# Optimization experiments

Measured on AMD Instinct MI355X. Metric: run time of the kernel, lower is better.

## Reference

```python
import jax, jax.numpy as jnp
import numpy as np

N_S, N_C, N_L = 100000, 20000, 5000
E_U, E_T = 2000000, 500000
D_S, D_C, D_L, H = 64, 32, 128, 128
N_LAYERS = 3  # num_layers=2 -> ModuleList holds 3 hetero layers


def _sage(h_src, h_dst, src_idx, dst_idx, W_self, W_neigh, b, n_dst):
    # DGL SAGEConv 'mean': fc_self(h_dst) + fc_neigh(mean of in-neighbor src feats) + bias
    summed = jax.ops.segment_sum(h_src[src_idx], dst_idx, num_segments=n_dst)  # [n_dst, d]
    deg = jax.ops.segment_sum(jnp.ones((src_idx.shape[0],), h_src.dtype), dst_idx, num_segments=n_dst)
    h_neigh = summed / jnp.maximum(deg, 1.0)[:, None]
    return h_dst @ W_self + h_neigh @ W_neigh + b


def setup_inputs() -> dict:
    key = jax.random.key(0)
    ks = jax.random.split(key, 24)
    s = 0.05
    inp = {
        'feat_student': jax.random.normal(ks[0], (N_S, D_S), jnp.float32),
        'feat_concept': jax.random.normal(ks[1], (N_C, D_C), jnp.float32),
        'feat_lecture': jax.random.normal(ks[2], (N_L, D_L), jnp.float32),
        'W_fs': jax.random.normal(ks[3], (D_S, H), jnp.float32) * s,
        'b_fs': jnp.zeros((H,), jnp.float32),
        'W_fc': jax.random.normal(ks[4], (D_C, H), jnp.float32) * s,
        'b_fc': jnp.zeros((H,), jnp.float32),
        'W_fl': jax.random.normal(ks[5], (D_L, H), jnp.float32) * s,
        'b_fl': jnp.zeros((H,), jnp.float32),
        # per-layer, per-relation SAGE params (all dims 128 so they stack)
        'W_self_u': jax.random.normal(ks[6], (N_LAYERS, H, H), jnp.float32) * s,
        'W_neigh_u': jax.random.normal(ks[7], (N_LAYERS, H, H), jnp.float32) * s,
        'b_u': jnp.zeros((N_LAYERS, H), jnp.float32),
        'W_self_t': jax.random.normal(ks[8], (N_LAYERS, H, H), jnp.float32) * s,
        'W_neigh_t': jax.random.normal(ks[9], (N_LAYERS, H, H), jnp.float32) * s,
        'b_t': jnp.zeros((N_LAYERS, H), jnp.float32),
        'und_src': jax.random.randint(ks[10], (E_U,), 0, N_S, jnp.int32),
        'und_dst': jax.random.randint(ks[11], (E_U,), 0, N_C, jnp.int32),
        'tea_src': jax.random.randint(ks[12], (E_T,), 0, N_L, jnp.int32),
        'tea_dst': jax.random.randint(ks[13], (E_T,), 0, N_C, jnp.int32),
    }
    return inp


def reference(feat_student, feat_concept, feat_lecture,
              W_fs, b_fs, W_fc, b_fc, W_fl, b_fl,
              W_self_u, W_neigh_u, b_u, W_self_t, W_neigh_t, b_t,
              und_src, und_dst, tea_src, tea_dst):
    # input projections per node type
    h_s = feat_student @ W_fs + b_fs
    h_c = feat_concept @ W_fc + b_fc
    h_l = feat_lecture @ W_fl + b_fl
    n_c = h_c.shape[0]
    for i in range(N_LAYERS):
        ou = _sage(h_s, h_c, und_src, und_dst, W_self_u[i], W_neigh_u[i], b_u[i], n_c)
        ot = _sage(h_l, h_c, tea_src, tea_dst, W_self_t[i], W_neigh_t[i], b_t[i], n_c)
        # HeteroGraphConv cross-relation aggregate: 'mean' on layer 0, default 'sum' after
        h_c = (ou + ot) * (0.5 if i == 0 else 1.0)
        if i != N_LAYERS - 1:
            h_c = jax.nn.relu(h_c)  # dropout is identity in eval mode
        # student/lecture are never destination types -> features pass through
    return h_c  # [N_C, 128] concept embeddings
```

## Files before the change

kernel.cpp:

```cpp
#include <hip/hip_runtime.h>
#include <hip/hip_bf16.h>
#include <cstdint>
#include <cstddef>

#define NS_ 100000
#define NC_ 20000
#define NL_ 5000
#define EU_ 2000000
#define ET_ 500000
#define H_  128

#define NBK_ 625
#define CHK_ 1954
#define UBLK_ 1024
#define TBLK_ 256
#define CAPU_ 3600
#define CAPT_ 1024
#define SEDGE_ 3712
#define SROW_ 640

typedef __attribute__((ext_vector_type(8))) short bs8;
typedef __attribute__((ext_vector_type(4))) float f32x4;
typedef __attribute__((ext_vector_type(2))) float v2f;

__device__ inline short bf_rne(float f) {
    unsigned u = __float_as_uint(f);
    u = (u + 0x7fffu + ((u >> 16) & 1u)) >> 16;
    return (short)u;
}
__device__ inline unsigned pack_bf16x2(float a, float b) {
    return ((unsigned)(unsigned short)bf_rne(a)) |
           (((unsigned)(unsigned short)bf_rne(b)) << 16);
}
__device__ inline float bflo(unsigned w) { return __uint_as_float(w << 16); }
__device__ inline float bfhi(unsigned w) { return __uint_as_float(w & 0xffff0000u); }

#define B_SCU UBLK_
#define B_SCT TBLK_
#define B_SCAT (B_SCU + B_SCT)
#define B_CVT 512
#define B_PACK 480
#define B_BC 2
#define B_WFC 16

__global__ __launch_bounds__(256) void count_kernel(
    const int* __restrict__ und_dst, const int* __restrict__ tea_dst,
    unsigned* __restrict__ CUm, unsigned* __restrict__ CTm)
{
    __shared__ unsigned cnt[768];
    const int b = blockIdx.x;
    const int tid = threadIdx.x;
    const bool isU = (b < B_SCU);
    const int blk = isU ? b : (b - B_SCU);
    const int nEdge = isU ? EU_ : ET_;
    const int* dstp = isU ? und_dst : tea_dst;
    unsigned* Cm = isU ? CUm : CTm;
    for (int i = tid; i < 768; i += 256) cnt[i] = 0;
    __syncthreads();
    const int start = blk * CHK_;
    const int end = min(start + CHK_, nEdge);
    for (int i = start + tid; i < end; i += 256)
        atomicAdd(&cnt[dstp[i] >> 5], 1u);
    __syncthreads();
    for (int i = tid; i < NBK_; i += 256)
        Cm[(size_t)blk * SROW_ + i] = cnt[i];
}

__global__ __launch_bounds__(256) void scan_kernel(
    const unsigned* __restrict__ CUm, const unsigned* __restrict__ CTm,
    unsigned* __restrict__ OUm, unsigned* __restrict__ OTm,
    unsigned* __restrict__ gcurU, unsigned* __restrict__ gcurT)
{
    __shared__ unsigned part[8][32];
    const int b = blockIdx.x;
    const int tid = threadIdx.x;
    const int s = tid >> 5;
    const int kl = tid & 31;
    const int k = b * 32 + kl;
    const bool ok = (k < NBK_);

    {
        unsigned run = 0;
        const int r0 = s * 128;
        if (ok) {
#pragma unroll 8
            for (int r = r0; r < r0 + 128; ++r)
                run += CUm[(size_t)r * SROW_ + k];
        }
        part[s][kl] = run;
        __syncthreads();
        unsigned base = 0;
        for (int s2 = 0; s2 < s; ++s2) base += part[s2][kl];
        if (ok && s == 7) gcurU[k] = base + run;
        if (ok) {
            unsigned acc = base;
#pragma unroll 8
            for (int r = r0; r < r0 + 128; ++r) {
                unsigned c = CUm[(size_t)r * SROW_ + k];
                OUm[(size_t)r * SROW_ + k] = acc;
                acc += c;
            }
        }
        __syncthreads();
    }
    {
        unsigned run = 0;
        const int r0 = s * 32;
        if (ok) {
#pragma unroll 8
            for (int r = r0; r < r0 + 32; ++r)
                run += CTm[(size_t)r * SROW_ + k];
        }
        part[s][kl] = run;
        __syncthreads();
        unsigned base = 0;
        for (int s2 = 0; s2 < s; ++s2) base += part[s2][kl];
        if (ok && s == 7) gcurT[k] = base + run;
        if (ok) {
            unsigned acc = base;
#pragma unroll 8
            for (int r = r0; r < r0 + 32; ++r) {
                unsigned c = CTm[(size_t)r * SROW_ + k];
                OTm[(size_t)r * SROW_ + k] = acc;
                acc += c;
            }
        }
    }
}

__global__ __launch_bounds__(256) void scatter_prep_kernel(
    const int* __restrict__ und_dst, const int* __restrict__ und_src,
    const int* __restrict__ tea_dst, const int* __restrict__ tea_src,
    const unsigned* __restrict__ CUm, const unsigned* __restrict__ CTm,
    const unsigned* __restrict__ OUm, const unsigned* __restrict__ OTm,
    unsigned* __restrict__ binnedU, unsigned* __restrict__ binnedT,
    const float* __restrict__ feat_s, unsigned* __restrict__ fs8,
    const float* __restrict__ feat_l, unsigned* __restrict__ flb,
    const float* __restrict__ Wsu, const float* __restrict__ Wnu,
    const float* __restrict__ Wst, const float* __restrict__ Wnt,
    const float* __restrict__ W_fs, const float* __restrict__ W_fl,
    short* __restrict__ WpL,
    const float* __restrict__ bu, const float* __restrict__ bt,
    const float* __restrict__ b_fs, const float* __restrict__ b_fl,
    float* __restrict__ bc,
    const float* __restrict__ W_fc, short* __restrict__ WpC)
{
    __shared__ unsigned smem[3776];
    const int b = blockIdx.x;
    const int tid = threadIdx.x;

    if (b < B_SCAT) {
        const bool isU = (b < B_SCU);
        const int blk = isU ? b : (b - B_SCU);
        const int nEdge = isU ? EU_ : ET_;
        const int* dstp = isU ? und_dst : tea_dst;
        const int* srcp = isU ? und_src : tea_src;
        const unsigned* Cm = isU ? CUm : CTm;
        const unsigned* Om = isU ? OUm : OTm;
        unsigned* binned = isU ? binnedU : binnedT;
        const unsigned cap = isU ? CAPU_ : CAPT_;
        unsigned* sed = smem;
        unsigned* cnt = smem + 1984;
        unsigned* pre = smem + 2752;
        unsigned* par = smem + 3520;

        unsigned Wr[3];
#pragma unroll
        for (int r = 0; r < 3; r++) {
            int k = r * 256 + tid;
            cnt[k] = (k < NBK_) ? Cm[(size_t)blk * SROW_ + k] : 0;
            Wr[r] = (k < NBK_) ? Om[(size_t)blk * SROW_ + k] : 0;
        }
        __syncthreads();
        unsigned c0 = cnt[3 * tid], c1 = cnt[3 * tid + 1], c2 = cnt[3 * tid + 2];
        unsigned s = c0 + c1 + c2;
        par[tid] = s;
        __syncthreads();
        unsigned sum = s;
        for (int d = 1; d < 256; d <<= 1) {
            unsigned x = (tid >= d) ? par[tid - d] : 0;
            __syncthreads();
            sum += x;
            par[tid] = sum;
            __syncthreads();
        }
        unsigned p = sum - s;
        pre[3 * tid] = p;
        pre[3 * tid + 1] = p + c0;
        pre[3 * tid + 2] = p + c0 + c1;
        __syncthreads();
#pragma unroll
        for (int r = 0; r < 3; r++) {
            int k = r * 256 + tid;
            if (k < NBK_) {
                unsigned L = cnt[k];
                unsigned W = Wr[r];
                if (W + L > cap) W = (L <= cap) ? cap - L : 0;
                cnt[k] = k * cap + W - pre[k];
            }
        }
        __syncthreads();
        const int start = blk * CHK_;
        const int end = min(start + CHK_, nEdge);
        for (int i = start + tid; i < end; i += 256) {
            int d = dstp[i];
            unsigned k = (unsigned)d >> 5;
            unsigned e = (unsigned)srcp[i] | ((unsigned)(d & 31) << 17) | (k << 22);
            unsigned pos = atomicAdd(&pre[k], 1u);
            sed[pos] = e;
        }
        __syncthreads();
        const int n = end - start;
        for (int i = tid; i < n; i += 256) {
            unsigned e = sed[i];
            binned[cnt[e >> 22] + i] = e & 0x3FFFFFu;
        }
    } else if (b < B_SCAT + B_CVT) {
        int i = (b - B_SCAT) * 256 + tid;
        const int stride = B_CVT * 256;
        const int nS = NS_ * 16;
        const int nTot = nS + NL_ * 64;
        for (; i < nTot; i += stride) {
            if (i < nS) {
                const float4 v = ((const float4*)feat_s)[i];
                unsigned r = __builtin_amdgcn_cvt_pk_fp8_f32(v.x, v.y, 0, false);
                r = __builtin_amdgcn_cvt_pk_fp8_f32(v.z, v.w, r, true);
                fs8[i] = r;
            } else {
                int j = i - nS;
                float2 v = ((const float2*)feat_l)[j];
                flb[j] = pack_bf16x2(v.x, v.y);
            }
        }
    } else if (b < B_SCAT + B_CVT + B_PACK) {
        int i = (b - B_SCAT - B_CVT) * 256 + tid;
        int j = i & 7;
        int lane = (i >> 3) & 63;
        int nt = (i >> 9) & 7;
        int ktAll = i >> 12;
        int l = ktAll / 10;
        int kt = ktAll - l * 10;
        int k = kt * 32 + (lane >> 4) * 8 + j;
        int n = nt * 16 + (lane & 15);
        const size_t WL = (size_t)l * H_ * H_;
        float v;
        if (k < 128) {
            v = Wsu[WL + k * H_ + n] + Wst[WL + k * H_ + n];
        } else if (k < 192) {
            int a = k - 128;
            v = 0.f;
            for (int t = 0; t < 128; t++) v += W_fs[a * H_ + t] * Wnu[WL + t * H_ + n];
        } else {
            int a = k - 192;
            v = 0.f;
            for (int t = 0; t < 128; t++) v += W_fl[a * H_ + t] * Wnt[WL + t * H_ + n];
        }
        WpL[i] = bf_rne(v);
    } else if (b < B_SCAT + B_CVT + B_PACK + B_BC) {
        int i = (b - B_SCAT - B_CVT - B_PACK) * 256 + tid;
        if (i < 3 * H_) {
            int l = i >> 7, c = i & 127;
            const size_t WL = (size_t)l * H_ * H_;
            float v = bu[i] + bt[i];
            for (int j2 = 0; j2 < 128; j2++)
                v += b_fs[j2] * Wnu[WL + j2 * H_ + c] + b_fl[j2] * Wnt[WL + j2 * H_ + c];
            bc[i] = v;
        }
    } else {
        int i = (b - (B_SCAT + B_CVT + B_PACK + B_BC)) * 256 + tid;
        int j = i & 7;
        int lane = (i >> 3) & 63;
        int nt = (i >> 9) & 7;
        int k = (lane >> 4) * 8 + j;
        int n = nt * 16 + (lane & 15);
        WpC[i] = bf_rne(W_fc[k * H_ + n]);
    }
}

__global__ __launch_bounds__(512) void agg_layers_kernel(
    const unsigned* __restrict__ gcurU, const unsigned* __restrict__ binnedU,
    const uint2* __restrict__ fs8,
    const unsigned* __restrict__ gcurT, const unsigned* __restrict__ binnedT,
    const uint4* __restrict__ flb4,
    const float* __restrict__ feat_c, const short* __restrict__ WpC,
    const float* __restrict__ b_fc,
    const short* __restrict__ WpL, const float* __restrict__ bc,
    float* __restrict__ out)
{
    __shared__ unsigned sedgeU[SEDGE_];
    __shared__ unsigned sedgeT[1024];
    __shared__ unsigned shU[32], soffU[33], scurU[32];
    __shared__ unsigned shT[32], soffT[33], scurT[32];
    __shared__ short tU[32 * 72];
    __shared__ short tT[32 * 136];
    __shared__ short tA[32 * 132];
    const int bb = blockIdx.x;
    const int tid = threadIdx.x;

    const int nU = min((int)gcurU[bb], CAPU_);
    const int nT = min((int)gcurT[bb], CAPT_);
    const size_t startU = (size_t)bb * CAPU_;
    const size_t startT = (size_t)bb * CAPT_;

    if (tid < 32) { shU[tid] = 0; shT[tid] = 0; }
    __syncthreads();
    for (int i = tid; i < nU; i += 512)
        atomicAdd(&shU[(binnedU[startU + i] >> 17) & 31], 1u);
    for (int i = tid; i < nT; i += 512)
        atomicAdd(&shT[(binnedT[startT + i] >> 17) & 31], 1u);
    __syncthreads();
    if (tid == 0) {
        unsigned r = 0;
        for (int j = 0; j < 32; j++) {
            unsigned v = shU[j]; soffU[j] = r; scurU[j] = r; r += v;
        }
        soffU[32] = r;
    }
    if (tid == 1) {
        unsigned r = 0;
        for (int j = 0; j < 32; j++) {
            unsigned v = shT[j]; soffT[j] = r; scurT[j] = r; r += v;
        }
        soffT[32] = r;
    }
    __syncthreads();
    for (int i = tid; i < nU; i += 512) {
        unsigned p = binnedU[startU + i];
        unsigned pos = atomicAdd(&scurU[(p >> 17) & 31], 1u);
        if (pos < SEDGE_) sedgeU[pos] = p & 0x1FFFFu;
    }
    for (int i = tid; i < nT; i += 512) {
        unsigned p = binnedT[startT + i];
        unsigned pos = atomicAdd(&scurT[(p >> 17) & 31], 1u);
        if (pos < 1024) sedgeT[pos] = p & 0x1FFFFu;
    }
    __syncthreads();

    const int g = tid >> 4;
    const int half = (tid >> 3) & 1;
    const int sub = tid & 7;

    {
        const int gs = (int)soffU[g];
        const int ge = (int)min(soffU[g + 1], (unsigned)SEDGE_);
        const int len = ge - gs;
        const int mid = gs + ((len + 1) >> 1);
        const int es = half ? mid : gs;
        const int ee = half ? ge : mid;
        const float inv = 1.f / (float)max(len, 1);
        float a[8];
#pragma unroll
        for (int i = 0; i < 8; i++) a[i] = 0.f;
        int e = es;
        for (; e + 4 <= ee; e += 4) {
            unsigned s0 = sedgeU[e], s1 = sedgeU[e + 1];
            unsigned s2 = sedgeU[e + 2], s3 = sedgeU[e + 3];
            uint2 w0 = fs8[(size_t)s0 * 8 + sub];
            uint2 w1 = fs8[(size_t)s1 * 8 + sub];
            uint2 w2 = fs8[(size_t)s2 * 8 + sub];
            uint2 w3 = fs8[(size_t)s3 * 8 + sub];
            v2f p0, p1, p2, p3;
            p0 = __builtin_amdgcn_cvt_pk_f32_fp8(w0.x, false);
            p1 = __builtin_amdgcn_cvt_pk_f32_fp8(w0.x, true);
            p2 = __builtin_amdgcn_cvt_pk_f32_fp8(w0.y, false);
            p3 = __builtin_amdgcn_cvt_pk_f32_fp8(w0.y, true);
            a[0] += p0.x; a[1] += p0.y; a[2] += p1.x; a[3] += p1.y;
            a[4] += p2.x; a[5] += p2.y; a[6] += p3.x; a[7] += p3.y;
            p0 = __builtin_amdgcn_cvt_pk_f32_fp8(w1.x, false);
            p1 = __builtin_amdgcn_cvt_pk_f32_fp8(w1.x, true);
            p2 = __builtin_amdgcn_cvt_pk_f32_fp8(w1.y, false);
            p3 = __builtin_amdgcn_cvt_pk_f32_fp8(w1.y, true);
            a[0] += p0.x; a[1] += p0.y; a[2] += p1.x; a[3] += p1.y;
            a[4] += p2.x; a[5] += p2.y; a[6] += p3.x; a[7] += p3.y;
            p0 = __builtin_amdgcn_cvt_pk_f32_fp8(w2.x, false);
            p1 = __builtin_amdgcn_cvt_pk_f32_fp8(w2.x, true);
            p2 = __builtin_amdgcn_cvt_pk_f32_fp8(w2.y, false);
            p3 = __builtin_amdgcn_cvt_pk_f32_fp8(w2.y, true);
            a[0] += p0.x; a[1] += p0.y; a[2] += p1.x; a[3] += p1.y;
            a[4] += p2.x; a[5] += p2.y; a[6] += p3.x; a[7] += p3.y;
            p0 = __builtin_amdgcn_cvt_pk_f32_fp8(w3.x, false);
            p1 = __builtin_amdgcn_cvt_pk_f32_fp8(w3.x, true);
            p2 = __builtin_amdgcn_cvt_pk_f32_fp8(w3.y, false);
            p3 = __builtin_amdgcn_cvt_pk_f32_fp8(w3.y, true);
            a[0] += p0.x; a[1] += p0.y; a[2] += p1.x; a[3] += p1.y;
            a[4] += p2.x; a[5] += p2.y; a[6] += p3.x; a[7] += p3.y;
        }
        for (; e < ee; e++) {
            uint2 w0 = fs8[(size_t)sedgeU[e] * 8 + sub];
            v2f p0 = __builtin_amdgcn_cvt_pk_f32_fp8(w0.x, false);
            v2f p1 = __builtin_amdgcn_cvt_pk_f32_fp8(w0.x, true);
            v2f p2 = __builtin_amdgcn_cvt_pk_f32_fp8(w0.y, false);
            v2f p3 = __builtin_amdgcn_cvt_pk_f32_fp8(w0.y, true);
            a[0] += p0.x; a[1] += p0.y; a[2] += p1.x; a[3] += p1.y;
            a[4] += p2.x; a[5] += p2.y; a[6] += p3.x; a[7] += p3.y;
        }
#pragma unroll
        for (int i = 0; i < 8; i++) a[i] += __shfl_xor(a[i], 8);
        if (half == 0) {
            unsigned* w = (unsigned*)tU + g * 36 + sub * 4;
            w[0] = pack_bf16x2(a[0] * inv, a[1] * inv);
            w[1] = pack_bf16x2(a[2] * inv, a[3] * inv);
            w[2] = pack_bf16x2(a[4] * inv, a[5] * inv);
            w[3] = pack_bf16x2(a[6] * inv, a[7] * inv);
        }
    }
    {
        const int gs = (int)soffT[g];
        const int ge = (int)min(soffT[g + 1], 1024u);
        const int len = ge - gs;
        const int mid = gs + ((len + 1) >> 1);
        const int es = half ? mid : gs;
        const int ee = half ? ge : mid;
        const float inv = 1.f / (float)max(len, 1);
        float a[16];
#pragma unroll
        for (int i = 0; i < 16; i++) a[i] = 0.f;
        int e = es;
        for (; e + 2 <= ee; e += 2) {
            unsigned s0 = sedgeT[e], s1 = sedgeT[e + 1];
            uint4 w0 = flb4[(size_t)s0 * 16 + sub * 2];
            uint4 w1 = flb4[(size_t)s0 * 16 + sub * 2 + 1];
            uint4 x0 = flb4[(size_t)s1 * 16 + sub * 2];
            uint4 x1 = flb4[(size_t)s1 * 16 + sub * 2 + 1];
            a[0] += bflo(w0.x); a[1] += bfhi(w0.x);
            a[2] += bflo(w0.y); a[3] += bfhi(w0.y);
            a[4] += bflo(w0.z); a[5] += bfhi(w0.z);
            a[6] += bflo(w0.w); a[7] += bfhi(w0.w);
            a[8]  += bflo(w1.x); a[9]  += bfhi(w1.x);
            a[10] += bflo(w1.y); a[11] += bfhi(w1.y);
            a[12] += bflo(w1.z); a[13] += bfhi(w1.z);
            a[14] += bflo(w1.w); a[15] += bfhi(w1.w);
            a[0] += bflo(x0.x); a[1] += bfhi(x0.x);
            a[2] += bflo(x0.y); a[3] += bfhi(x0.y);
            a[4] += bflo(x0.z); a[5] += bfhi(x0.z);
            a[6] += bflo(x0.w); a[7] += bfhi(x0.w);
            a[8]  += bflo(x1.x); a[9]  += bfhi(x1.x);
            a[10] += bflo(x1.y); a[11] += bfhi(x1.y);
            a[12] += bflo(x1.z); a[13] += bfhi(x1.z);
            a[14] += bflo(x1.w); a[15] += bfhi(x1.w);
        }
        if (e < ee) {
            unsigned src = sedgeT[e];
            uint4 w0 = flb4[(size_t)src * 16 + sub * 2];
            uint4 w1 = flb4[(size_t)src * 16 + sub * 2 + 1];
            a[0] += bflo(w0.x); a[1] += bfhi(w0.x);
            a[2] += bflo(w0.y); a[3] += bfhi(w0.y);
            a[4] += bflo(w0.z); a[5] += bfhi(w0.z);
            a[6] += bflo(w0.w); a[7] += bfhi(w0.w);
            a[8]  += bflo(w1.x); a[9]  += bfhi(w1.x);
            a[10] += bflo(w1.y); a[11] += bfhi(w1.y);
            a[12] += bflo(w1.z); a[13] += bfhi(w1.z);
            a[14] += bflo(w1.w); a[15] += bfhi(w1.w);
        }
#pragma unroll
        for (int i = 0; i < 16; i++) a[i] += __shfl_xor(a[i], 8);
        if (half == 0) {
            unsigned* w = (unsigned*)tT + g * 68 + sub * 8;
            w[0] = pack_bf16x2(a[0] * inv, a[1] * inv);
            w[1] = pack_bf16x2(a[2] * inv, a[3] * inv);
            w[2] = pack_bf16x2(a[4] * inv, a[5] * inv);
            w[3] = pack_bf16x2(a[6] * inv, a[7] * inv);
            w[4] = pack_bf16x2(a[8] * inv, a[9] * inv);
            w[5] = pack_bf16x2(a[10] * inv, a[11] * inv);
            w[6] = pack_bf16x2(a[12] * inv, a[13] * inv);
            w[7] = pack_bf16x2(a[14] * inv, a[15] * inv);
        }
    }
    __syncthreads();

    const int lane = tid & 63;
    const int wv = tid >> 6;
    const int gr = wv >> 2;
    const int h = wv & 3;
    const int q = lane >> 4;
    const int m = lane & 15;
    const int rL = gr * 16 + m;
    const int rA = bb * 32 + rL;

    bs8 fuF[2], ftF[4], hcF[4];
#pragma unroll
    for (int kt = 0; kt < 2; kt++)
        fuF[kt] = *(const bs8*)(tU + rL * 72 + kt * 32 + q * 8);
#pragma unroll
    for (int kt = 0; kt < 4; kt++)
        ftF[kt] = *(const bs8*)(tT + rL * 136 + kt * 32 + q * 8);

    f32x4 acc[2];
#pragma unroll
    for (int i = 0; i < 2; i++) acc[i] = (f32x4){0.f, 0.f, 0.f, 0.f};
    {
        const float* xp = feat_c + (size_t)rA * 32 + q * 8;
        float4 xa = *(const float4*)xp;
        float4 xb = *(const float4*)(xp + 4);
        bs8 af;
        af[0] = bf_rne(xa.x); af[1] = bf_rne(xa.y); af[2] = bf_rne(xa.z); af[3] = bf_rne(xa.w);
        af[4] = bf_rne(xb.x); af[5] = bf_rne(xb.y); af[6] = bf_rne(xb.z); af[7] = bf_rne(xb.w);
#pragma unroll
        for (int nt = 0; nt < 2; nt++) {
            int ntg = h * 2 + nt;
            bs8 bfr = *(const bs8*)(WpC + ((size_t)ntg * 64 + lane) * 8);
            acc[nt] = __builtin_amdgcn_mfma_f32_16x16x32_bf16(af, bfr, acc[nt], 0, 0, 0);
        }
    }
#pragma unroll
    for (int nt = 0; nt < 2; nt++) {
        int col = (h * 2 + nt) * 16 + m;
        float bv = b_fc[col];
#pragma unroll
        for (int r = 0; r < 4; r++)
            tA[(gr * 16 + q * 4 + r) * 132 + col] = bf_rne(acc[nt][r] + bv);
    }
    __syncthreads();
#pragma unroll
    for (int kt = 0; kt < 4; kt++)
        hcF[kt] = *(const bs8*)(tA + rL * 132 + kt * 32 + q * 8);
    __syncthreads();

#pragma unroll
    for (int l = 0; l < 3; l++) {
#pragma unroll
        for (int i = 0; i < 2; i++) acc[i] = (f32x4){0.f, 0.f, 0.f, 0.f};
        const short* wl = WpL + (size_t)l * 40960;
#pragma unroll
        for (int kt = 0; kt < 10; kt++) {
            bs8 af = (kt < 4) ? hcF[kt] : ((kt < 6) ? fuF[kt - 4] : ftF[kt - 6]);
            const short* wp = wl + (size_t)kt * 4096;
#pragma unroll
            for (int nt = 0; nt < 2; nt++) {
                int ntg = h * 2 + nt;
                bs8 bfr = *(const bs8*)(wp + ((size_t)ntg * 64 + lane) * 8);
                acc[nt] = __builtin_amdgcn_mfma_f32_16x16x32_bf16(af, bfr, acc[nt], 0, 0, 0);
            }
        }
        const float scale = (l == 0) ? 0.5f : 1.0f;
        const float* bl = bc + l * H_;
        if (l < 2) {
#pragma unroll
            for (int nt = 0; nt < 2; nt++) {
                int col = (h * 2 + nt) * 16 + m;
                float bv = bl[col];
#pragma unroll
                for (int r = 0; r < 4; r++)
                    tA[(gr * 16 + q * 4 + r) * 132 + col] =
                        bf_rne(fmaxf((acc[nt][r] + bv) * scale, 0.f));
            }
            __syncthreads();
#pragma unroll
            for (int kt = 0; kt < 4; kt++)
                hcF[kt] = *(const bs8*)(tA + rL * 132 + kt * 32 + q * 8);
            __syncthreads();
        } else {
#pragma unroll
            for (int nt = 0; nt < 2; nt++) {
                int col = (h * 2 + nt) * 16 + m;
                float bv = bl[col];
#pragma unroll
                for (int r = 0; r < 4; r++) {
                    int row = bb * 32 + gr * 16 + q * 4 + r;
                    out[(size_t)row * H_ + col] = (acc[nt][r] + bv) * scale;
                }
            }
        }
    }
}

extern "C" void kernel_launch(void* const* d_in, const int* in_sizes, int n_in,
                              void* d_out, int out_size, void* d_ws, size_t ws_size,
                              hipStream_t stream)
{
    (void)in_sizes; (void)n_in; (void)out_size; (void)ws_size;
    const float* feat_s = (const float*)d_in[0];
    const float* feat_c = (const float*)d_in[1];
    const float* feat_l = (const float*)d_in[2];
    const float* W_fs = (const float*)d_in[3];
    const float* b_fs = (const float*)d_in[4];
    const float* W_fc = (const float*)d_in[5];
    const float* b_fc = (const float*)d_in[6];
    const float* W_fl = (const float*)d_in[7];
    const float* b_fl = (const float*)d_in[8];
    const float* W_self_u  = (const float*)d_in[9];
    const float* W_neigh_u = (const float*)d_in[10];
    const float* b_u = (const float*)d_in[11];
    const float* W_self_t  = (const float*)d_in[12];
    const float* W_neigh_t = (const float*)d_in[13];
    const float* b_t = (const float*)d_in[14];
    const int* und_src = (const int*)d_in[15];
    const int* und_dst = (const int*)d_in[16];
    const int* tea_src = (const int*)d_in[17];
    const int* tea_dst = (const int*)d_in[18];
    float* out = (float*)d_out;

    char* ws = (char*)d_ws;
    size_t o = 0;
    auto alloc = [&](size_t bytes) -> char* {
        char* p = ws + o;
        o += (bytes + 255) & ~(size_t)255;
        return p;
    };
    unsigned* fs8  = (unsigned*)alloc((size_t)NS_ * 16 * 4);
    unsigned* flb  = (unsigned*)alloc((size_t)NL_ * 64 * 4);
    short* WpL = (short*)alloc((size_t)3 * 10 * 8 * 64 * 8 * 2);
    short* WpC = (short*)alloc((size_t)8 * 64 * 8 * 2);
    float* bc  = (float*)alloc((size_t)3 * H_ * 4);
    unsigned* gcurU = (unsigned*)alloc((size_t)NBK_ * 4);
    unsigned* gcurT = (unsigned*)alloc((size_t)NBK_ * 4);
    unsigned* binnedU = (unsigned*)alloc((size_t)NBK_ * CAPU_ * 4);
    unsigned* binnedT = (unsigned*)alloc((size_t)NBK_ * CAPT_ * 4);
    unsigned* CUm = (unsigned*)alloc((size_t)UBLK_ * SROW_ * 4);
    unsigned* OUm = (unsigned*)alloc((size_t)UBLK_ * SROW_ * 4);
    unsigned* CTm = (unsigned*)alloc((size_t)TBLK_ * SROW_ * 4);
    unsigned* OTm = (unsigned*)alloc((size_t)TBLK_ * SROW_ * 4);

    count_kernel<<<B_SCAT, 256, 0, stream>>>(und_dst, tea_dst, CUm, CTm);

    scan_kernel<<<20, 256, 0, stream>>>(CUm, CTm, OUm, OTm, gcurU, gcurT);

    scatter_prep_kernel<<<B_SCAT + B_CVT + B_PACK + B_BC + B_WFC, 256, 0, stream>>>(
        und_dst, und_src, tea_dst, tea_src,
        CUm, CTm, OUm, OTm, binnedU, binnedT,
        feat_s, fs8, feat_l, flb,
        W_self_u, W_neigh_u, W_self_t, W_neigh_t, W_fs, W_fl, WpL,
        b_u, b_t, b_fs, b_fl, bc,
        W_fc, WpC);

    agg_layers_kernel<<<NBK_, 512, 0, stream>>>(
        gcurU, binnedU, (const uint2*)fs8,
        gcurT, binnedT, (const uint4*)flb,
        feat_c, WpC, b_fc, WpL, bc, out);
}
```

Before: 199.1 us.

## Double agg kernel block to 1024 threads, splitting edges and MFMA tiles further

```diff
diff --git a/kernel.cpp b/kernel.cpp
--- a/kernel.cpp
+++ b/kernel.cpp
@@ -277,7 +277,7 @@
     }
 }
 
-__global__ __launch_bounds__(512) void agg_layers_kernel(
+__global__ __launch_bounds__(1024) void agg_layers_kernel(
     const unsigned* __restrict__ gcurU, const unsigned* __restrict__ binnedU,
     const uint2* __restrict__ fs8,
     const unsigned* __restrict__ gcurT, const unsigned* __restrict__ binnedT,
@@ -302,12 +302,20 @@
     const size_t startU = (size_t)bb * CAPU_;
     const size_t startT = (size_t)bb * CAPT_;
 
+    unsigned evU[4];
+#pragma unroll
+    for (int r = 0; r < 4; r++) {
+        int i = tid + r * 1024;
+        evU[r] = (i < nU) ? binnedU[startU + i] : 0xFFFFFFFFu;
+    }
+    unsigned evT = (tid < nT) ? binnedT[startT + tid] : 0xFFFFFFFFu;
+
     if (tid < 32) { shU[tid] = 0; shT[tid] = 0; }
     __syncthreads();
-    for (int i = tid; i < nU; i += 512)
-        atomicAdd(&shU[(binnedU[startU + i] >> 17) & 31], 1u);
-    for (int i = tid; i < nT; i += 512)
-        atomicAdd(&shT[(binnedT[startT + i] >> 17) & 31], 1u);
+#pragma unroll
+    for (int r = 0; r < 4; r++)
+        if (evU[r] != 0xFFFFFFFFu) atomicAdd(&shU[(evU[r] >> 17) & 31], 1u);
+    if (evT != 0xFFFFFFFFu) atomicAdd(&shT[(evT >> 17) & 31], 1u);
     __syncthreads();
     if (tid == 0) {
         unsigned r = 0;
@@ -324,29 +332,29 @@
         soffT[32] = r;
     }
     __syncthreads();
-    for (int i = tid; i < nU; i += 512) {
-        unsigned p = binnedU[startU + i];
-        unsigned pos = atomicAdd(&scurU[(p >> 17) & 31], 1u);
-        if (pos < SEDGE_) sedgeU[pos] = p & 0x1FFFFu;
-    }
-    for (int i = tid; i < nT; i += 512) {
-        unsigned p = binnedT[startT + i];
-        unsigned pos = atomicAdd(&scurT[(p >> 17) & 31], 1u);
-        if (pos < 1024) sedgeT[pos] = p & 0x1FFFFu;
-    }
-    __syncthreads();
-
-    const int g = tid >> 4;
-    const int half = (tid >> 3) & 1;
+#pragma unroll
+    for (int r = 0; r < 4; r++)
+        if (evU[r] != 0xFFFFFFFFu) {
+            unsigned pos = atomicAdd(&scurU[(evU[r] >> 17) & 31], 1u);
+            if (pos < SEDGE_) sedgeU[pos] = evU[r] & 0x1FFFFu;
+        }
+    if (evT != 0xFFFFFFFFu) {
+        unsigned pos = atomicAdd(&scurT[(evT >> 17) & 31], 1u);
+        if (pos < 1024) sedgeT[pos] = evT & 0x1FFFFu;
+    }
+    __syncthreads();
+
+    const int g = tid >> 5;
+    const int quarter = (tid >> 3) & 3;
     const int sub = tid & 7;
 
     {
         const int gs = (int)soffU[g];
         const int ge = (int)min(soffU[g + 1], (unsigned)SEDGE_);
         const int len = ge - gs;
-        const int mid = gs + ((len + 1) >> 1);
-        const int es = half ? mid : gs;
-        const int ee = half ? ge : mid;
+        const int qlen = len >> 2;
+        const int es = gs + quarter * qlen;
+        const int ee = (quarter == 3) ? ge : (es + qlen);
         const float inv = 1.f / (float)max(len, 1);
         float a[8];
 #pragma unroll
@@ -395,8 +403,11 @@
             a[4] += p2.x; a[5] += p2.y; a[6] += p3.x; a[7] += p3.y;
         }
 #pragma unroll
-        for (int i = 0; i < 8; i++) a[i] += __shfl_xor(a[i], 8);
-        if (half == 0) {
+        for (int i = 0; i < 8; i++) {
+            a[i] += __shfl_xor(a[i], 8);
+            a[i] += __shfl_xor(a[i], 16);
+        }
+        if (quarter == 0) {
             unsigned* w = (unsigned*)tU + g * 36 + sub * 4;
             w[0] = pack_bf16x2(a[0] * inv, a[1] * inv);
             w[1] = pack_bf16x2(a[2] * inv, a[3] * inv);
@@ -408,9 +419,9 @@
         const int gs = (int)soffT[g];
         const int ge = (int)min(soffT[g + 1], 1024u);
         const int len = ge - gs;
-        const int mid = gs + ((len + 1) >> 1);
-        const int es = half ? mid : gs;
-        const int ee = half ? ge : mid;
+        const int qlen = len >> 2;
+        const int es = gs + quarter * qlen;
+        const int ee = (quarter == 3) ? ge : (es + qlen);
         const float inv = 1.f / (float)max(len, 1);
         float a[16];
 #pragma unroll
@@ -453,8 +464,11 @@
             a[14] += bflo(w1.w); a[15] += bfhi(w1.w);
         }
 #pragma unroll
-        for (int i = 0; i < 16; i++) a[i] += __shfl_xor(a[i], 8);
-        if (half == 0) {
+        for (int i = 0; i < 16; i++) {
+            a[i] += __shfl_xor(a[i], 8);
+            a[i] += __shfl_xor(a[i], 16);
+        }
+        if (quarter == 0) {
             unsigned* w = (unsigned*)tT + g * 68 + sub * 8;
             w[0] = pack_bf16x2(a[0] * inv, a[1] * inv);
             w[1] = pack_bf16x2(a[2] * inv, a[3] * inv);
@@ -470,8 +484,8 @@
 
     const int lane = tid & 63;
     const int wv = tid >> 6;
-    const int gr = wv >> 2;
-    const int h = wv & 3;
+    const int gr = wv >> 3;
+    const int h = wv & 7;
     const int q = lane >> 4;
     const int m = lane & 15;
     const int rL = gr * 16 + m;
@@ -485,9 +499,7 @@
     for (int kt = 0; kt < 4; kt++)
         ftF[kt] = *(const bs8*)(tT + rL * 136 + kt * 32 + q * 8);
 
-    f32x4 acc[2];
-#pragma unroll
-    for (int i = 0; i < 2; i++) acc[i] = (f32x4){0.f, 0.f, 0.f, 0.f};
+    f32x4 acc = (f32x4){0.f, 0.f, 0.f, 0.f};
     {
         const float* xp = feat_c + (size_t)rA * 32 + q * 8;
         float4 xa = *(const float4*)xp;
@@ -495,20 +507,15 @@
         bs8 af;
         af[0] = bf_rne(xa.x); af[1] = bf_rne(xa.y); af[2] = bf_rne(xa.z); af[3] = bf_rne(xa.w);
         af[4] = bf_rne(xb.x); af[5] = bf_rne(xb.y); af[6] = bf_rne(xb.z); af[7] = bf_rne(xb.w);
-#pragma unroll
-        for (int nt = 0; nt < 2; nt++) {
-            int ntg = h * 2 + nt;
-            bs8 bfr = *(const bs8*)(WpC + ((size_t)ntg * 64 + lane) * 8);
-            acc[nt] = __builtin_amdgcn_mfma_f32_16x16x32_bf16(af, bfr, acc[nt], 0, 0, 0);
-        }
-    }
-#pragma unroll
-    for (int nt = 0; nt < 2; nt++) {
-        int col = (h * 2 + nt) * 16 + m;
+        bs8 bfr = *(const bs8*)(WpC + ((size_t)h * 64 + lane) * 8);
+        acc = __builtin_amdgcn_mfma_f32_16x16x32_bf16(af, bfr, acc, 0, 0, 0);
+    }
+    {
+        int col = h * 16 + m;
         float bv = b_fc[col];
 #pragma unroll
         for (int r = 0; r < 4; r++)
-            tA[(gr * 16 + q * 4 + r) * 132 + col] = bf_rne(acc[nt][r] + bv);
+            tA[(gr * 16 + q * 4 + r) * 132 + col] = bf_rne(acc[r] + bv);
     }
     __syncthreads();
 #pragma unroll
@@ -518,47 +525,35 @@
 
 #pragma unroll
     for (int l = 0; l < 3; l++) {
-#pragma unroll
-        for (int i = 0; i < 2; i++) acc[i] = (f32x4){0.f, 0.f, 0.f, 0.f};
+        acc = (f32x4){0.f, 0.f, 0.f, 0.f};
         const short* wl = WpL + (size_t)l * 40960;
 #pragma unroll
         for (int kt = 0; kt < 10; kt++) {
             bs8 af = (kt < 4) ? hcF[kt] : ((kt < 6) ? fuF[kt - 4] : ftF[kt - 6]);
-            const short* wp = wl + (size_t)kt * 4096;
-#pragma unroll
-            for (int nt = 0; nt < 2; nt++) {
-                int ntg = h * 2 + nt;
-                bs8 bfr = *(const bs8*)(wp + ((size_t)ntg * 64 + lane) * 8);
-                acc[nt] = __builtin_amdgcn_mfma_f32_16x16x32_bf16(af, bfr, acc[nt], 0, 0, 0);
-            }
+            bs8 bfr = *(const bs8*)(wl + (size_t)kt * 4096 + ((size_t)h * 64 + lane) * 8);
+            acc = __builtin_amdgcn_mfma_f32_16x16x32_bf16(af, bfr, acc, 0, 0, 0);
         }
         const float scale = (l == 0) ? 0.5f : 1.0f;
         const float* bl = bc + l * H_;
         if (l < 2) {
-#pragma unroll
-            for (int nt = 0; nt < 2; nt++) {
-                int col = (h * 2 + nt) * 16 + m;
-                float bv = bl[col];
-#pragma unroll
-                for (int r = 0; r < 4; r++)
-                    tA[(gr * 16 + q * 4 + r) * 132 + col] =
-                        bf_rne(fmaxf((acc[nt][r] + bv) * scale, 0.f));
-            }
+            int col = h * 16 + m;
+            float bv = bl[col];
+#pragma unroll
+            for (int r = 0; r < 4; r++)
+                tA[(gr * 16 + q * 4 + r) * 132 + col] =
+                    bf_rne(fmaxf((acc[r] + bv) * scale, 0.f));
             __syncthreads();
 #pragma unroll
             for (int kt = 0; kt < 4; kt++)
                 hcF[kt] = *(const bs8*)(tA + rL * 132 + kt * 32 + q * 8);
             __syncthreads();
         } else {
-#pragma unroll
-            for (int nt = 0; nt < 2; nt++) {
-                int col = (h * 2 + nt) * 16 + m;
-                float bv = bl[col];
-#pragma unroll
-                for (int r = 0; r < 4; r++) {
-                    int row = bb * 32 + gr * 16 + q * 4 + r;
-                    out[(size_t)row * H_ + col] = (acc[nt][r] + bv) * scale;
-                }
+            int col = h * 16 + m;
+            float bv = bl[col];
+#pragma unroll
+            for (int r = 0; r < 4; r++) {
+                int row = bb * 32 + gr * 16 + q * 4 + r;
+                out[(size_t)row * H_ + col] = (acc[r] + bv) * scale;
             }
         }
     }
@@ -623,7 +618,7 @@
         b_u, b_t, b_fs, b_fl, bc,
         W_fc, WpC);
 
-    agg_layers_kernel<<<NBK_, 512, 0, stream>>>(
+    agg_layers_kernel<<<NBK_, 1024, 0, stream>>>(
         gcurU, binnedU, (const uint2*)fs8,
         gcurT, binnedT, (const uint4*)flb,
         feat_c, WpC, b_fc, WpL, bc, out);
```

Result: slower. 207.5 us (+4.2%).
